# Kernel tuning notes

Hardware: AMD Instinct MI355X
Metric: run time of the kernel (lower is better)

The kernel has to match this reference:

```python
import jax, jax.numpy as jnp
import numpy as np
import math

N_EMBD = 1024
N_HEAD = 16
D_HEAD = N_EMBD // N_HEAD
LCOMP = 576 // 2  # 288
B, T = 4, 2048

def setup_inputs() -> dict:
    key = jax.random.key(0)
    k1, k2, k3, k4 = jax.random.split(key, 4)
    x = jax.random.normal(k1, (B, T, N_EMBD), dtype=jnp.float32)
    Wdkv = jax.random.normal(k2, (B, T, LCOMP), dtype=jnp.float32)
    # nn.Linear(n_embd, LCompression): weight [LCOMP, n_embd], bias [LCOMP]
    Wd_w = jax.random.normal(k3, (LCOMP, N_EMBD), dtype=jnp.float32) * (1.0 / math.sqrt(N_EMBD))
    Wd_b = jax.random.normal(k4, (LCOMP,), dtype=jnp.float32) * 0.01
    return {"x": x, "Wdkv": Wdkv, "Wd_w": Wd_w, "Wd_b": Wd_b}

def reference(x, Wdkv, Wd_w, Wd_b):
    b, t, c = x.shape
    # q: [b, t, LCOMP]
    q = jnp.einsum('btc,lc->btl', x, Wd_w) + Wd_b
    # scores: [b, t, t] -- query positions attend over latent rows of Wdkv
    h = jnp.einsum('btl,bsl->bts', q, Wdkv) / math.sqrt(D_HEAD)
    causal = jnp.tril(jnp.ones((t, t), dtype=bool))  # True where allowed
    h = jnp.where(causal[None, :, :], h, -jnp.inf)
    y = jax.nn.softmax(h, axis=-1)
    # output: [b, t, LCOMP]
    return jnp.einsum('bts,bsl->btl', y, Wdkv)
```

## Files before the change

kernel.cpp:

```cpp
#include <hip/hip_runtime.h>

#define TT 2048
#define LL 288
#define CC 1024
#define SLOTB2 74752

typedef __attribute__((ext_vector_type(8))) short bf16x8;
typedef __attribute__((ext_vector_type(4))) float f32x4;
typedef __attribute__((ext_vector_type(4))) unsigned int u32x4;
typedef __attribute__((ext_vector_type(2))) unsigned int u32x2;
typedef __attribute__((ext_vector_type(4))) short s16x4;

__device__ __forceinline__ unsigned short f2bf(float f) {
  unsigned u = __float_as_uint(f);
  u += 0x7fffu + ((u >> 16) & 1u);
  return (unsigned short)(u >> 16);
}

__device__ __forceinline__ u32x2 pack4(f32x4 v) {
  u32x2 p;
  p.x = (unsigned)f2bf(v.x) | ((unsigned)f2bf(v.y) << 16);
  p.y = (unsigned)f2bf(v.z) | ((unsigned)f2bf(v.w) << 16);
  return p;
}

__device__ __forceinline__ f32x4 mfma16(bf16x8 a, bf16x8 b, f32x4 c) {
  return __builtin_amdgcn_mfma_f32_16x16x32_bf16(a, b, c, 0, 0, 0);
}

__device__ __forceinline__ bf16x8 as_bf(u32x4 u) {
  return __builtin_bit_cast(bf16x8, u);
}

__device__ __forceinline__ unsigned cvtpk(float lo, float hi) {
  unsigned d;
  asm("v_cvt_pk_bf16_f32 %0, %1, %2" : "=v"(d) : "v"(lo), "v"(hi));
  return d;
}

typedef __attribute__((address_space(3))) const unsigned short* lds_cptr;
typedef __attribute__((address_space(1))) const void* gvp;
typedef __attribute__((address_space(3))) void* svp;

__device__ __forceinline__ s16x4 tr16(const void* p) {
  s16x4 r;
  lds_cptr lp = (lds_cptr)p;
  asm volatile("ds_read_b64_tr_b16 %0, %1" : "=v"(r) : "v"(lp));
  return r;
}

__device__ __forceinline__ void gll16(const void* g, void* l) {
  __builtin_amdgcn_global_load_lds((gvp)g, (svp)l, 16, 0, 0);
}

__global__ __launch_bounds__(256) void tobf16(const float* __restrict__ x,
                                              const float* __restrict__ wdkv,
                                              const float* __restrict__ ww,
                                              unsigned short* __restrict__ xB,
                                              unsigned short* __restrict__ wdkvT,
                                              unsigned short* __restrict__ wwB) {
  long i8 = (long)blockIdx.x * 256 + threadIdx.x;
  if (i8 < 1048576L) {
    f32x4 a = *(const f32x4*)(x + i8 * 8);
    f32x4 c = *(const f32x4*)(x + i8 * 8 + 4);
    u32x2 p0 = pack4(a), p1 = pack4(c);
    u32x4 o;
    o.x = p0.x; o.y = p0.y; o.z = p1.x; o.w = p1.y;
    *(u32x4*)(xB + i8 * 8) = o;
  } else if (i8 < 1085440L) {
    long k = i8 - 1048576L;
    f32x4 a = *(const f32x4*)(ww + k * 8);
    f32x4 c = *(const f32x4*)(ww + k * 8 + 4);
    u32x2 p0 = pack4(a), p1 = pack4(c);
    u32x4 o;
    o.x = p0.x; o.y = p0.y; o.z = p1.x; o.w = p1.y;
    *(u32x4*)(wwB + k * 8) = o;
  } else {
    long k = i8 - 1085440L;
    int b = (int)(k / 73728);
    int rem = (int)(k % 73728);
    int srow = rem / 36;
    int l8 = rem - srow * 36;
    int st = srow >> 6;
    int s = srow & 63;
    int j = (l8 >> 1) * 2 + (s >> 5);
    int lane = ((s & 31) >> 2) * 8 + (s & 3) * 2 + (l8 & 1);
    f32x4 a = *(const f32x4*)(wdkv + k * 8);
    f32x4 c = *(const f32x4*)(wdkv + k * 8 + 4);
    u32x2 p0 = pack4(a), p1 = pack4(c);
    u32x4 o;
    o.x = p0.x; o.y = p0.y; o.z = p1.x; o.w = p1.y;
    *(u32x4*)((char*)wdkvT + (((long)(b * 32 + st) * 36 + j) << 10) + lane * 16) = o;
  }
}

__global__ __launch_bounds__(256, 4) void qproj(const unsigned short* __restrict__ xB,
                                                const unsigned short* __restrict__ wwB,
                                                const float* __restrict__ Wb,
                                                unsigned short* __restrict__ q) {
  __shared__ unsigned short xl[2][64 * 64];
  __shared__ unsigned short wl[2][96 * 64];
  const int tid = threadIdx.x;
  const int lane = tid & 63;
  const int w = tid >> 6;
  const int g = lane >> 4;
  const int r = lane & 15;
  const int m0 = (blockIdx.x / 3) * 64;
  const int c0 = (blockIdx.x % 3) * 96;

  const int o_i = (lane >> 3) * 2048 + (((lane & 7) * 16) ^ ((lane >> 3) << 4));

  f32x4 acc[6];
#pragma unroll
  for (int i = 0; i < 6; ++i) acc[i] = (f32x4)0.0f;

  const char* xsrc = (const char*)xB + (long)m0 * 2048;
  const char* wsrc = (const char*)wwB + (long)c0 * 2048;

#define QPROJ_ISSUE(kb2, cb)                                            \
  {                                                                     \
    char* xd = (char*)&xl[cb][0];                                       \
    char* wd = (char*)&wl[cb][0];                                       \
    _Pragma("unroll") for (int jj = 0; jj < 2; ++jj) {                  \
      int j = 2 * w + jj;                                               \
      gll16(xsrc + (long)j * 16384 + (kb2) + o_i, xd + j * 1024);       \
    }                                                                   \
    _Pragma("unroll") for (int jj = 0; jj < 3; ++jj) {                  \
      int j = 3 * w + jj;                                               \
      gll16(wsrc + (long)j * 16384 + (kb2) + o_i, wd + j * 1024);       \
    }                                                                   \
  }

  QPROJ_ISSUE(0, 0);
  for (int ks = 0; ks < 16; ++ks) {
    const int cb = ks & 1;
    if (ks < 15) {
      QPROJ_ISSUE((ks + 1) * 128, cb ^ 1);
      asm volatile("s_waitcnt vmcnt(5)" ::: "memory");
    } else {
      asm volatile("s_waitcnt vmcnt(0)" ::: "memory");
    }
    __builtin_amdgcn_s_barrier();
    __builtin_amdgcn_sched_barrier(0);
    const char* xlb = (const char*)&xl[cb][0];
    const char* wlb = (const char*)&wl[cb][0];
#pragma unroll
    for (int kc = 0; kc < 2; ++kc) {
      int koff = kc * 64 + g * 16;
      bf16x8 a = as_bf(*(const u32x4*)(xlb + (16 * w + r) * 128 + (koff ^ ((r & 7) << 4))));
#pragma unroll
      for (int nf = 0; nf < 6; ++nf) {
        int l = nf * 16 + r;
        bf16x8 bb = as_bf(*(const u32x4*)(wlb + l * 128 + (koff ^ ((l & 7) << 4))));
        acc[nf] = mfma16(a, bb, acc[nf]);
      }
    }
    __builtin_amdgcn_sched_barrier(0);
    __builtin_amdgcn_s_barrier();
    __builtin_amdgcn_sched_barrier(0);
  }
  const int rowb = m0 + 16 * w + 4 * g;
#pragma unroll
  for (int nf = 0; nf < 6; ++nf) {
    int col = c0 + nf * 16 + r;
    float bias = Wb[col];
#pragma unroll
    for (int e = 0; e < 4; ++e) {
      float qv = (acc[nf][e] + bias) * 0.125f;
      q[(long)(rowb + e) * LL + col] = f2bf(qv);
    }
  }
}

__global__ __launch_bounds__(512, 2) void attn(const unsigned short* __restrict__ wdkvT,
                                               const unsigned short* __restrict__ q,
                                               float* __restrict__ out,
                                               char* __restrict__ partial,
                                               int CH, int SPB) {
  __shared__ unsigned short Vt[2][18 * 16 * 64];
  const int tid = threadIdx.x;
  const int lane = tid & 63;
  const int w = tid >> 6;
  const int g = lane >> 4;
  const int r = lane & 15;

  const int bid = blockIdx.x;
  const int b = bid / SPB;
  int rem = bid - b * SPB;
  int t = 0, base = 0, nch = 1;
  for (;;) {
    nch = (2 * t + 2 + CH - 1) / CH;
    if (rem < base + nch) break;
    base += nch;
    ++t;
  }
  const int c = rem - base;
  const bool direct = (nch == 1);
  const int q0 = t * 128;
  const int st0 = c * CH;
  const int st1 = min((c + 1) * CH, 2 * t + 2);

  char* vt0 = (char*)&Vt[0][0];
  char* vt1 = (char*)&Vt[1][0];

  const char* wsrcT = (const char*)wdkvT + (long)b * 32 * 36864;

  bf16x8 qf[9];
  {
    const long qrow = (long)b * TT + q0 + 16 * w + r;
#pragma unroll
    for (int kc = 0; kc < 9; ++kc)
      qf[kc] = as_bf(*(const u32x4*)(q + qrow * LL + kc * 32 + 8 * g));
  }

  f32x4 o[18];
#pragma unroll
  for (int i = 0; i < 18; ++i) o[i] = (f32x4)0.0f;
  float mr = -1e30f, lr = 0.0f;

#define ATTN_ISSUE(st_, dst_)                                          \
  {                                                                    \
    const char* srcT = wsrcT + (long)(st_) * 36864;                    \
    _Pragma("unroll") for (int jj = 0; jj < 5; ++jj) {                 \
      int j = w + 8 * jj;                                              \
      if (j < 36) gll16(srcT + j * 1024 + lane * 16, (dst_) + j * 1024);\
    }                                                                  \
  }

  const int rq = q0 + 16 * w + r;
  const int srcA = r + 32 * (g & 1);
  const int srcB = srcA + 16;
  const bool gsel = (g & 2) != 0;

  ATTN_ISSUE(st0, vt0);
  for (int st = st0; st < st1; ++st) {
    const int sb = st * 64;
    const int cbi = (st - st0) & 1;
    char* vtb = cbi ? vt1 : vt0;
    char* vtn = cbi ? vt0 : vt1;
    asm volatile("s_waitcnt vmcnt(0)" ::: "memory");
    __builtin_amdgcn_s_barrier();
    __builtin_amdgcn_sched_barrier(0);
    if (st + 1 < st1) ATTN_ISSUE(st + 1, vtn);
    f32x4 sa[4];
#pragma unroll
    for (int i = 0; i < 4; ++i) sa[i] = (f32x4)0.0f;
    __builtin_amdgcn_s_setprio(1);
#pragma unroll
    for (int kc = 0; kc < 9; ++kc) {
      const int lblk2048 = (2 * kc + (g >> 1)) * 2048;
      const int lrem16 = (g & 1) * 16;
#pragma unroll
      for (int sf = 0; sf < 4; ++sf) {
        bf16x8 vv = as_bf(*(const u32x4*)(vtb + lblk2048 + (4 * sf + (r >> 2)) * 128 + (r & 3) * 32 + lrem16));
        sa[sf] = mfma16(vv, qf[kc], sa[sf]);
      }
    }
    __builtin_amdgcn_s_setprio(0);
    float tm = -1e30f;
#pragma unroll
    for (int sf = 0; sf < 4; ++sf)
#pragma unroll
      for (int e = 0; e < 4; ++e) {
        int sg = sb + 16 * sf + 4 * g + e;
        if (sg > rq) sa[sf][e] = -1e30f;
        tm = fmaxf(tm, sa[sf][e]);
      }
    tm = fmaxf(tm, __shfl_xor(tm, 16));
    tm = fmaxf(tm, __shfl_xor(tm, 32));
    const float mn = fmaxf(mr, tm);
    const float al = __expf(mr - mn);
    mr = mn;
    float rs = 0.0f;
#pragma unroll
    for (int sf = 0; sf < 4; ++sf)
#pragma unroll
      for (int e = 0; e < 4; ++e) {
        float pv = __expf(sa[sf][e] - mn);
        sa[sf][e] = pv;
        rs += pv;
      }
    rs += __shfl_xor(rs, 16);
    rs += __shfl_xor(rs, 32);
    lr = lr * al + rs;
    float alr[4];
#pragma unroll
    for (int e = 0; e < 4; ++e) alr[e] = __shfl(al, 4 * g + e);
#pragma unroll
    for (int nf = 0; nf < 18; ++nf)
#pragma unroll
      for (int e = 0; e < 4; ++e) o[nf][e] *= alr[e];
    unsigned pk[4][2];
#pragma unroll
    for (int sf = 0; sf < 4; ++sf) {
      pk[sf][0] = cvtpk(sa[sf][0], sa[sf][1]);
      pk[sf][1] = cvtpk(sa[sf][2], sa[sf][3]);
    }
#pragma unroll
    for (int kc2 = 0; kc2 < 2; ++kc2) {
      int xa0 = __shfl((int)pk[2 * kc2 + 0][0], srcA);
      int xb0 = __shfl((int)pk[2 * kc2 + 1][0], srcA);
      int xa1 = __shfl((int)pk[2 * kc2 + 0][1], srcA);
      int xb1 = __shfl((int)pk[2 * kc2 + 1][1], srcA);
      int ya0 = __shfl((int)pk[2 * kc2 + 0][0], srcB);
      int yb0 = __shfl((int)pk[2 * kc2 + 1][0], srcB);
      int ya1 = __shfl((int)pk[2 * kc2 + 0][1], srcB);
      int yb1 = __shfl((int)pk[2 * kc2 + 1][1], srcB);
      u32x4 pd;
      pd.x = (unsigned)(gsel ? xb0 : xa0);
      pd.y = (unsigned)(gsel ? xb1 : xa1);
      pd.z = (unsigned)(gsel ? yb0 : ya0);
      pd.w = (unsigned)(gsel ? yb1 : ya1);
      bf16x8 pa = as_bf(pd);
      const int base0 = kc2 * 1024 + g * 256 + r * 8;
#pragma unroll
      for (int gg = 0; gg < 6; ++gg) {
        s16x4 tq[6];
#pragma unroll
        for (int i = 0; i < 3; ++i) {
          int nf = gg * 3 + i;
          tq[2 * i] = tr16(vtb + nf * 2048 + base0);
          tq[2 * i + 1] = tr16(vtb + nf * 2048 + base0 + 128);
        }
        asm volatile("s_waitcnt lgkmcnt(0)" ::: "memory");
        __builtin_amdgcn_sched_barrier(0);
        __builtin_amdgcn_s_setprio(1);
#pragma unroll
        for (int i = 0; i < 3; ++i) {
          int nf = gg * 3 + i;
          s16x4 t0 = tq[2 * i], t1 = tq[2 * i + 1];
          bf16x8 bb;
          bb[0] = t0[0]; bb[1] = t0[1]; bb[2] = t0[2]; bb[3] = t0[3];
          bb[4] = t1[0]; bb[5] = t1[1]; bb[6] = t1[2]; bb[7] = t1[3];
          o[nf] = mfma16(pa, bb, o[nf]);
        }
        __builtin_amdgcn_s_setprio(0);
      }
    }
  }
  if (direct) {
    float lrr[4];
#pragma unroll
    for (int e = 0; e < 4; ++e) lrr[e] = __shfl(lr, 4 * g + e);
    const long trow = (long)b * TT + q0 + 16 * w + 4 * g;
#pragma unroll
    for (int nf = 0; nf < 18; ++nf) {
      int col = 16 * nf + r;
#pragma unroll
      for (int e = 0; e < 4; ++e)
        out[(trow + e) * LL + col] = o[nf][e] / lrr[e];
    }
  } else {
    char* sp = partial + (size_t)(b * SPB + rem) * SLOTB2;
    if (g == 0) {
      ((float*)sp)[16 * w + r] = mr;
      ((float*)(sp + 512))[16 * w + r] = lr;
    }
#pragma unroll
    for (int p = 0; p < 9; ++p) {
      u32x2 a0 = pack4(o[2 * p]);
      u32x2 a1 = pack4(o[2 * p + 1]);
      u32x4 v;
      v.x = a0.x; v.y = a0.y; v.z = a1.x; v.w = a1.y;
      *(u32x4*)(sp + 1024 + p * 8192 + tid * 16) = v;
    }
  }
}

__global__ __launch_bounds__(512) void reduce_k(const char* __restrict__ partial,
                                                float* __restrict__ out,
                                                int CH, int SPB, int NMT) {
  const int bid = blockIdx.x;
  const int nfl = bid % 9;
  const int rest = bid / 9;
  const int b = rest / NMT;
  int idx = rest % NMT;
  int t = 0, base = 0, nch = 1;
  for (;;) {
    nch = (2 * t + 2 + CH - 1) / CH;
    if (nch > 1) {
      if (idx == 0) break;
      --idx;
    }
    base += nch;
    ++t;
  }
  const char* sp0 = partial + (size_t)(b * SPB + base) * SLOTB2;

  const int tid = threadIdx.x;
  const int w = tid >> 6;
  const int g = (tid & 63) >> 4;
  const int r = tid & 15;
  const int row0 = 16 * w + 4 * g;

  float M[4], Lx[4], acc[8];
#pragma unroll
  for (int e = 0; e < 4; ++e) { M[e] = -1e30f; Lx[e] = 0.0f; }
#pragma unroll
  for (int k = 0; k < 8; ++k) acc[k] = 0.0f;

  for (int i = 0; i < nch; ++i) {
    const char* sp = sp0 + (size_t)i * SLOTB2;
    const float* mv = (const float*)sp;
    const float* lv = (const float*)(sp + 512);
    u32x4 v = *(const u32x4*)(sp + 1024 + nfl * 8192 + tid * 16);
    const unsigned short* pu = (const unsigned short*)&v;
    float fo[4], fi[4];
#pragma unroll
    for (int e = 0; e < 4; ++e) {
      float mi = mv[row0 + e];
      float mn = fmaxf(M[e], mi);
      fo[e] = __expf(M[e] - mn);
      fi[e] = __expf(mi - mn);
      Lx[e] = Lx[e] * fo[e] + fi[e] * lv[row0 + e];
      M[e] = mn;
    }
#pragma unroll
    for (int k = 0; k < 8; ++k)
      acc[k] = acc[k] * fo[k & 3] + fi[k & 3] * __uint_as_float((unsigned)pu[k] << 16);
  }
#pragma unroll
  for (int k = 0; k < 8; ++k) {
    int row = row0 + (k & 3);
    int col = 16 * (2 * nfl + (k >> 2)) + r;
    out[((size_t)b * TT + t * 128 + row) * LL + col] = acc[k] / Lx[k & 3];
  }
}

extern "C" void kernel_launch(void* const* d_in, const int* in_sizes, int n_in,
                              void* d_out, int out_size, void* d_ws, size_t ws_size,
                              hipStream_t stream) {
  const float* x = (const float*)d_in[0];
  const float* Wdkv = (const float*)d_in[1];
  const float* Ww = (const float*)d_in[2];
  const float* Wb = (const float*)d_in[3];
  float* outp = (float*)d_out;

  char* ws = (char*)d_ws;
  unsigned short* qB = (unsigned short*)ws;
  unsigned short* xB = (unsigned short*)(ws + 4718592);
  unsigned short* wdkvT = (unsigned short*)(ws + 21495808);
  unsigned short* wwB = (unsigned short*)(ws + 26214400);
  char* partialB = ws + 26804224;

  int CH = 32, SPB = 16;
  const int chs[4] = {5, 8, 16, 32};
  for (int ci = 0; ci < 4; ++ci) {
    int ch = chs[ci];
    int spb = 0;
    for (int t = 0; t < 16; ++t) spb += (2 * t + 2 + ch - 1) / ch;
    if (26804224 + (size_t)4 * spb * SLOTB2 <= ws_size) { CH = ch; SPB = spb; break; }
  }
  int NMT = 0;
  for (int t = 0; t < 16; ++t)
    if ((2 * t + 2 + CH - 1) / CH > 1) ++NMT;

  tobf16<<<5392, 256, 0, stream>>>(x, Wdkv, Ww, xB, wdkvT, wwB);
  qproj<<<384, 256, 0, stream>>>(xB, wwB, Wb, qB);
  attn<<<4 * SPB, 512, 0, stream>>>(wdkvT, qB, outp, partialB, CH, SPB);
  if (NMT > 0) reduce_k<<<4 * NMT * 9, 512, 0, stream>>>(partialB, outp, CH, SPB, NMT);
}
```

Baseline: 64.26 us.

## Fuse x fp32-to-bf16 conversion into qproj and software-pipeline PV LDS reads

The separate pass that converted x to bf16 in the workspace is removed. qproj now loads fp32 x directly into registers, packs it to bf16 and writes it to swizzled LDS, double-buffered against the MFMA work, which drops an extra global write and read of x. The attention PV loop is also restructured into a flat 36-step pipeline with a three-slot rotating buffer of transposed LDS reads and partial lgkmcnt waits, so reads overlap with MFMAs. The qproj x path now uses register loads instead of direct global-to-LDS loads and waits on vmcnt(0) every iteration, which may expose load latency.

```diff
diff --git a/kernel.cpp b/kernel.cpp
--- a/kernel.cpp
+++ b/kernel.cpp
@@ -53,22 +53,13 @@
   __builtin_amdgcn_global_load_lds((gvp)g, (svp)l, 16, 0, 0);
 }
 
-__global__ __launch_bounds__(256) void tobf16(const float* __restrict__ x,
-                                              const float* __restrict__ wdkv,
+__global__ __launch_bounds__(256) void tobf16(const float* __restrict__ wdkv,
                                               const float* __restrict__ ww,
-                                              unsigned short* __restrict__ xB,
                                               unsigned short* __restrict__ wdkvT,
                                               unsigned short* __restrict__ wwB) {
   long i8 = (long)blockIdx.x * 256 + threadIdx.x;
-  if (i8 < 1048576L) {
-    f32x4 a = *(const f32x4*)(x + i8 * 8);
-    f32x4 c = *(const f32x4*)(x + i8 * 8 + 4);
-    u32x2 p0 = pack4(a), p1 = pack4(c);
-    u32x4 o;
-    o.x = p0.x; o.y = p0.y; o.z = p1.x; o.w = p1.y;
-    *(u32x4*)(xB + i8 * 8) = o;
-  } else if (i8 < 1085440L) {
-    long k = i8 - 1048576L;
+  if (i8 < 36864L) {
+    long k = i8;
     f32x4 a = *(const f32x4*)(ww + k * 8);
     f32x4 c = *(const f32x4*)(ww + k * 8 + 4);
     u32x2 p0 = pack4(a), p1 = pack4(c);
@@ -76,7 +67,7 @@
     o.x = p0.x; o.y = p0.y; o.z = p1.x; o.w = p1.y;
     *(u32x4*)(wwB + k * 8) = o;
   } else {
-    long k = i8 - 1085440L;
+    long k = i8 - 36864L;
     int b = (int)(k / 73728);
     int rem = (int)(k % 73728);
     int srow = rem / 36;
@@ -94,7 +85,7 @@
   }
 }
 
-__global__ __launch_bounds__(256, 4) void qproj(const unsigned short* __restrict__ xB,
+__global__ __launch_bounds__(256, 4) void qproj(const float* __restrict__ x,
                                                 const unsigned short* __restrict__ wwB,
                                                 const float* __restrict__ Wb,
                                                 unsigned short* __restrict__ q) {
@@ -110,38 +101,55 @@
 
   const int o_i = (lane >> 3) * 2048 + (((lane & 7) * 16) ^ ((lane >> 3) << 4));
 
+  const int mi = tid >> 2;
+  const int kq = (tid & 3) * 16;
+  const float* xrow = x + (long)(m0 + mi) * CC + kq;
+  const int xb0 = mi * 128 + (((kq * 2) + 0) ^ ((mi & 7) << 4));
+  const int xb1 = mi * 128 + (((kq * 2) + 16) ^ ((mi & 7) << 4));
+
   f32x4 acc[6];
 #pragma unroll
   for (int i = 0; i < 6; ++i) acc[i] = (f32x4)0.0f;
 
-  const char* xsrc = (const char*)xB + (long)m0 * 2048;
   const char* wsrc = (const char*)wwB + (long)c0 * 2048;
 
-#define QPROJ_ISSUE(kb2, cb)                                            \
+#define QPROJ_W_ISSUE(kb2, cb)                                          \
   {                                                                     \
-    char* xd = (char*)&xl[cb][0];                                       \
     char* wd = (char*)&wl[cb][0];                                       \
-    _Pragma("unroll") for (int jj = 0; jj < 2; ++jj) {                  \
-      int j = 2 * w + jj;                                               \
-      gll16(xsrc + (long)j * 16384 + (kb2) + o_i, xd + j * 1024);       \
-    }                                                                   \
     _Pragma("unroll") for (int jj = 0; jj < 3; ++jj) {                  \
       int j = 3 * w + jj;                                               \
       gll16(wsrc + (long)j * 16384 + (kb2) + o_i, wd + j * 1024);       \
     }                                                                   \
   }
 
-  QPROJ_ISSUE(0, 0);
+  {
+    f32x4 a0 = *(const f32x4*)(xrow + 0);
+    f32x4 a1 = *(const f32x4*)(xrow + 4);
+    f32x4 a2 = *(const f32x4*)(xrow + 8);
+    f32x4 a3 = *(const f32x4*)(xrow + 12);
+    QPROJ_W_ISSUE(0, 0);
+    u32x2 pA = pack4(a0), pB = pack4(a1), pC = pack4(a2), pD = pack4(a3);
+    u32x4 v0, v1;
+    v0.x = pA.x; v0.y = pA.y; v0.z = pB.x; v0.w = pB.y;
+    v1.x = pC.x; v1.y = pC.y; v1.z = pD.x; v1.w = pD.y;
+    *(u32x4*)((char*)&xl[0][0] + xb0) = v0;
+    *(u32x4*)((char*)&xl[0][0] + xb1) = v1;
+  }
+  asm volatile("s_waitcnt vmcnt(0) lgkmcnt(0)" ::: "memory");
+  __builtin_amdgcn_s_barrier();
+  __builtin_amdgcn_sched_barrier(0);
+
   for (int ks = 0; ks < 16; ++ks) {
     const int cb = ks & 1;
+    f32x4 a0, a1, a2, a3;
     if (ks < 15) {
-      QPROJ_ISSUE((ks + 1) * 128, cb ^ 1);
-      asm volatile("s_waitcnt vmcnt(5)" ::: "memory");
-    } else {
-      asm volatile("s_waitcnt vmcnt(0)" ::: "memory");
-    }
-    __builtin_amdgcn_s_barrier();
-    __builtin_amdgcn_sched_barrier(0);
+      const float* xs = xrow + (ks + 1) * 64;
+      a0 = *(const f32x4*)(xs + 0);
+      a1 = *(const f32x4*)(xs + 4);
+      a2 = *(const f32x4*)(xs + 8);
+      a3 = *(const f32x4*)(xs + 12);
+      QPROJ_W_ISSUE((ks + 1) * 128, cb ^ 1);
+    }
     const char* xlb = (const char*)&xl[cb][0];
     const char* wlb = (const char*)&wl[cb][0];
 #pragma unroll
@@ -155,6 +163,17 @@
         acc[nf] = mfma16(a, bb, acc[nf]);
       }
     }
+    if (ks < 15) {
+      asm volatile("s_waitcnt vmcnt(0)" ::: "memory");
+      u32x2 pA = pack4(a0), pB = pack4(a1), pC = pack4(a2), pD = pack4(a3);
+      u32x4 v0, v1;
+      v0.x = pA.x; v0.y = pA.y; v0.z = pB.x; v0.w = pB.y;
+      v1.x = pC.x; v1.y = pC.y; v1.z = pD.x; v1.w = pD.y;
+      char* xd = (char*)&xl[cb ^ 1][0];
+      *(u32x4*)(xd + xb0) = v0;
+      *(u32x4*)(xd + xb1) = v1;
+    }
+    asm volatile("s_waitcnt lgkmcnt(0)" ::: "memory");
     __builtin_amdgcn_sched_barrier(0);
     __builtin_amdgcn_s_barrier();
     __builtin_amdgcn_sched_barrier(0);
@@ -296,6 +315,7 @@
       pk[sf][0] = cvtpk(sa[sf][0], sa[sf][1]);
       pk[sf][1] = cvtpk(sa[sf][2], sa[sf][3]);
     }
+    bf16x8 paK0, paK1;
 #pragma unroll
     for (int kc2 = 0; kc2 < 2; ++kc2) {
       int xa0 = __shfl((int)pk[2 * kc2 + 0][0], srcA);
@@ -311,32 +331,38 @@
       pd.y = (unsigned)(gsel ? xb1 : xa1);
       pd.z = (unsigned)(gsel ? yb0 : ya0);
       pd.w = (unsigned)(gsel ? yb1 : ya1);
-      bf16x8 pa = as_bf(pd);
-      const int base0 = kc2 * 1024 + g * 256 + r * 8;
-#pragma unroll
-      for (int gg = 0; gg < 6; ++gg) {
-        s16x4 tq[6];
-#pragma unroll
-        for (int i = 0; i < 3; ++i) {
-          int nf = gg * 3 + i;
-          tq[2 * i] = tr16(vtb + nf * 2048 + base0);
-          tq[2 * i + 1] = tr16(vtb + nf * 2048 + base0 + 128);
-        }
+      if (kc2 == 0) paK0 = as_bf(pd); else paK1 = as_bf(pd);
+    }
+    asm volatile("" : "+v"(paK0), "+v"(paK1));
+    s16x4 tq[3][2];
+#define PV_ISSUE(c_, sl_)                                                   \
+    {                                                                       \
+      const char* ap = vtb + ((c_) % 18) * 2048 + ((c_) / 18) * 1024 + g * 256 + r * 8; \
+      tq[sl_][0] = tr16(ap);                                                \
+      tq[sl_][1] = tr16(ap + 128);                                          \
+    }
+    __builtin_amdgcn_s_setprio(1);
+    PV_ISSUE(0, 0);
+    PV_ISSUE(1, 1);
+#pragma unroll
+    for (int cc2 = 0; cc2 < 36; ++cc2) {
+      if (cc2 < 34) {
+        PV_ISSUE(cc2 + 2, (cc2 + 2) % 3);
+        asm volatile("s_waitcnt lgkmcnt(4)" ::: "memory");
+      } else if (cc2 == 34) {
+        asm volatile("s_waitcnt lgkmcnt(2)" ::: "memory");
+      } else {
         asm volatile("s_waitcnt lgkmcnt(0)" ::: "memory");
-        __builtin_amdgcn_sched_barrier(0);
-        __builtin_amdgcn_s_setprio(1);
-#pragma unroll
-        for (int i = 0; i < 3; ++i) {
-          int nf = gg * 3 + i;
-          s16x4 t0 = tq[2 * i], t1 = tq[2 * i + 1];
-          bf16x8 bb;
-          bb[0] = t0[0]; bb[1] = t0[1]; bb[2] = t0[2]; bb[3] = t0[3];
-          bb[4] = t1[0]; bb[5] = t1[1]; bb[6] = t1[2]; bb[7] = t1[3];
-          o[nf] = mfma16(pa, bb, o[nf]);
-        }
-        __builtin_amdgcn_s_setprio(0);
       }
-    }
+      __builtin_amdgcn_sched_barrier(0);
+      const int nf = cc2 % 18;
+      s16x4 t0 = tq[cc2 % 3][0], t1 = tq[cc2 % 3][1];
+      bf16x8 bb;
+      bb[0] = t0[0]; bb[1] = t0[1]; bb[2] = t0[2]; bb[3] = t0[3];
+      bb[4] = t1[0]; bb[5] = t1[1]; bb[6] = t1[2]; bb[7] = t1[3];
+      o[nf] = mfma16((cc2 < 18) ? paK0 : paK1, bb, o[nf]);
+    }
+    __builtin_amdgcn_s_setprio(0);
   }
   if (direct) {
     float lrr[4];
@@ -438,10 +464,9 @@
 
   char* ws = (char*)d_ws;
   unsigned short* qB = (unsigned short*)ws;
-  unsigned short* xB = (unsigned short*)(ws + 4718592);
-  unsigned short* wdkvT = (unsigned short*)(ws + 21495808);
-  unsigned short* wwB = (unsigned short*)(ws + 26214400);
-  char* partialB = ws + 26804224;
+  unsigned short* wdkvT = (unsigned short*)(ws + 4718592);
+  unsigned short* wwB = (unsigned short*)(ws + 9437184);
+  char* partialB = ws + 10027008;
 
   int CH = 32, SPB = 16;
   const int chs[4] = {5, 8, 16, 32};
@@ -449,14 +474,14 @@
     int ch = chs[ci];
     int spb = 0;
     for (int t = 0; t < 16; ++t) spb += (2 * t + 2 + ch - 1) / ch;
-    if (26804224 + (size_t)4 * spb * SLOTB2 <= ws_size) { CH = ch; SPB = spb; break; }
+    if (10027008 + (size_t)4 * spb * SLOTB2 <= ws_size) { CH = ch; SPB = spb; break; }
   }
   int NMT = 0;
   for (int t = 0; t < 16; ++t)
     if ((2 * t + 2 + CH - 1) / CH > 1) ++NMT;
 
-  tobf16<<<5392, 256, 0, stream>>>(x, Wdkv, Ww, xB, wdkvT, wwB);
-  qproj<<<384, 256, 0, stream>>>(xB, wwB, Wb, qB);
+  tobf16<<<1296, 256, 0, stream>>>(Wdkv, Ww, wdkvT, wwB);
+  qproj<<<384, 256, 0, stream>>>(x, wwB, Wb, qB);
   attn<<<4 * SPB, 512, 0, stream>>>(wdkvT, qB, outp, partialB, CH, SPB);
   if (NMT > 0) reduce_k<<<4 * NMT * 9, 512, 0, stream>>>(partialB, outp, CH, SPB, NMT);
 }
```

Measured after the change: 70.67 us. 10.0% more time.
